# Kernel optimization log

Hardware: AMD Instinct MI355X
Metric: run time of the kernel (lower is better)

The kernel has to match this reference:

```python
import jax, jax.numpy as jnp
import numpy as np

B, S, D = 4, 2048, 256
H = 8
HD = D // H
FF = 1024
LEN_M1 = 513


def _layer_norm(x, gamma, beta, eps=1e-5):
    m = jnp.mean(x, axis=-1, keepdims=True)
    v = jnp.var(x, axis=-1, keepdims=True)
    return (x - m) * jax.lax.rsqrt(v + eps) * gamma + beta


def setup_inputs() -> dict:
    key = jax.random.key(0)
    ks = jax.random.split(key, 16)
    s = 0.02  # init scale for weights
    return {
        "src": jax.random.normal(ks[0], (B, S, D), dtype=jnp.float32),
        "Wq": jax.random.normal(ks[1], (D, D), dtype=jnp.float32) * s,
        "bq": jnp.zeros((D,), dtype=jnp.float32),
        "Wk": jax.random.normal(ks[2], (D, D), dtype=jnp.float32) * s,
        "bk": jnp.zeros((D,), dtype=jnp.float32),
        "Wv": jax.random.normal(ks[3], (D, D), dtype=jnp.float32) * s,
        "bv": jnp.zeros((D,), dtype=jnp.float32),
        "Wo": jax.random.normal(ks[4], (D, D), dtype=jnp.float32) * s,
        "bo": jnp.zeros((D,), dtype=jnp.float32),
        "W1": jax.random.normal(ks[5], (FF, D), dtype=jnp.float32) * s,
        "b1": jnp.zeros((FF,), dtype=jnp.float32),
        "W2": jax.random.normal(ks[6], (D, FF), dtype=jnp.float32) * s,
        "b2": jnp.zeros((D,), dtype=jnp.float32),
        "g1": jnp.ones((D,), dtype=jnp.float32),
        "be1": jnp.zeros((D,), dtype=jnp.float32),
        "g2": jnp.ones((D,), dtype=jnp.float32),
        "be2": jnp.zeros((D,), dtype=jnp.float32),
        "len_m1": LEN_M1,
    }


def reference(src, Wq, bq, Wk, bk, Wv, bv, Wo, bo, W1, b1, W2, b2, g1, be1, g2, be2, len_m1):
    Bb, Ss, Dd = src.shape
    hd = Dd // H
    # projections (torch Linear: x @ W.T + b), split heads -> [B,H,S,hd]
    q = (src @ Wq.T + bq).reshape(Bb, Ss, H, hd).transpose(0, 2, 1, 3)
    k = (src @ Wk.T + bk).reshape(Bb, Ss, H, hd).transpose(0, 2, 1, 3)
    v = (src @ Wv.T + bv).reshape(Bb, Ss, H, hd).transpose(0, 2, 1, 3)
    scores = jnp.einsum("bhqd,bhkd->bhqk", q, k) / np.sqrt(hd).astype(np.float32)
    # causal mask + global prefix block: masked where j > i OR (i < len_m1 and j >= len_m1)
    i = jnp.arange(Ss)[:, None]
    j = jnp.arange(Ss)[None, :]
    mask = (j > i) | ((i < len_m1) & (j >= len_m1))
    scores = jnp.where(mask, -jnp.inf, scores)
    attn = jax.nn.softmax(scores, axis=-1)
    ao = jnp.einsum("bhqk,bhkd->bhqd", attn, v).transpose(0, 2, 1, 3).reshape(Bb, Ss, Dd)
    src2 = _layer_norm(src + (ao @ Wo.T + bo), g1, be1)
    ff = jax.nn.gelu(src2 @ W1.T + b1, approximate=False) @ W2.T + b2
    return _layer_norm(src2 + ff, g2, be2)
```

## Files before the change

kernel.cpp:

```cpp
#include <hip/hip_runtime.h>
#include <math.h>

#define NB 4
#define NS 2048
#define ND 256
#define NH 8
#define NHD 32
#define NFF 1024
#define NM (NB*NS)
#define KPAD 40
#define VSP 72
#define VTP 72
#define AS 264
#define QSCALE 0.2550181657f

typedef __attribute__((ext_vector_type(4))) short short4v;
typedef __attribute__((ext_vector_type(8))) short short8v;
typedef __attribute__((ext_vector_type(4))) float f32x4;
typedef unsigned short us;

__device__ __forceinline__ us f2bf(float f){
  union { float f; unsigned u; } c; c.f = f;
  unsigned u = c.u + 0x7fffu + ((c.u >> 16) & 1u);
  return (us)(u >> 16);
}

__device__ __forceinline__ float wsum(float v){
  #pragma unroll
  for(int o=32;o>0;o>>=1) v += __shfl_xor(v,o);
  return v;
}

__global__ __launch_bounds__(256) void prep_kernel(
    const float* __restrict__ src,
    const float* __restrict__ Wq, const float* __restrict__ Wk, const float* __restrict__ Wv,
    const float* __restrict__ Wo, const float* __restrict__ W1, const float* __restrict__ W2,
    const float* __restrict__ bq,
    us* __restrict__ X, us* __restrict__ Wqkvb, us* __restrict__ Wob,
    us* __restrict__ W1b, us* __restrict__ W2b, float* __restrict__ bqs){
  unsigned bid = blockIdx.x;
  if (bid == 1408){ bqs[threadIdx.x] = bq[threadIdx.x]*QSCALE; return; }
  unsigned u = bid*256u + threadIdx.x;
  const float* sp; us* dp; float sc = 1.f;
  if (u < 262144u){ sp = src + (size_t)u*8; dp = X + (size_t)u*8; }
  else {
    unsigned v = u - 262144u;
    if      (v <  8192u){ sp = Wq + (size_t)v*8;            dp = Wqkvb + (size_t)v*8;            sc = QSCALE; }
    else if (v < 16384u){ sp = Wk + (size_t)(v- 8192u)*8;   dp = Wqkvb + 65536 + (size_t)(v- 8192u)*8; }
    else if (v < 24576u){ sp = Wv + (size_t)(v-16384u)*8;   dp = Wqkvb + 131072 + (size_t)(v-16384u)*8; }
    else if (v < 32768u){ sp = Wo + (size_t)(v-24576u)*8;   dp = Wob + (size_t)(v-24576u)*8; }
    else if (v < 65536u){ sp = W1 + (size_t)(v-32768u)*8;   dp = W1b + (size_t)(v-32768u)*8; }
    else               { sp = W2 + (size_t)(v-65536u)*8;    dp = W2b + (size_t)(v-65536u)*8; }
  }
  float4 a = *(const float4*)sp, b = *(const float4*)(sp+4);
  short8v o;
  o[0]=(short)f2bf(a.x*sc); o[1]=(short)f2bf(a.y*sc); o[2]=(short)f2bf(a.z*sc); o[3]=(short)f2bf(a.w*sc);
  o[4]=(short)f2bf(b.x*sc); o[5]=(short)f2bf(b.y*sc); o[6]=(short)f2bf(b.z*sc); o[7]=(short)f2bf(b.w*sc);
  *(short8v*)dp = o;
}

template<int KTOT, int EPI>
__global__ __launch_bounds__(256) void gemm_kernel(
    const us* __restrict__ A, const us* __restrict__ W,
    const float* __restrict__ bias0, const float* __restrict__ bias1, const float* __restrict__ bias2,
    const float* __restrict__ resid,
    us* __restrict__ outb, us* __restrict__ outv, float* __restrict__ outf){
  __shared__ us Asl[64*AS];
  const int t = threadIdx.x, l = t&63, wv = t>>6;
  const int lx = l&15, lw = l>>4;
  const int m0 = blockIdx.y*64;
  const int n0 = blockIdx.x*128 + wv*32;

  f32x4 acc[4][2];
  #pragma unroll
  for(int mb=0;mb<4;mb++)
    #pragma unroll
    for(int nb=0;nb<2;nb++) acc[mb][nb] = (f32x4){0.f,0.f,0.f,0.f};

  for (int kc = 0; kc < KTOT; kc += 256){
    __syncthreads();
    #pragma unroll
    for (int it=0; it<8; it++){
      int idx = it*256 + t;
      int r = idx>>5, c = idx&31;
      *(short8v*)&Asl[r*AS + c*8] = *(const short8v*)(A + (size_t)(m0+r)*KTOT + kc + c*8);
    }
    __syncthreads();
    short8v bf[2][8];
    #pragma unroll
    for (int nb=0; nb<2; nb++)
      #pragma unroll
      for (int ks=0; ks<8; ks++)
        bf[nb][ks] = *(const short8v*)(W + (size_t)(n0 + nb*16 + lx)*KTOT + kc + ks*32 + 8*lw);
    #pragma unroll
    for (int ks=0; ks<8; ks++){
      short8v af[4];
      #pragma unroll
      for (int mb=0; mb<4; mb++)
        af[mb] = *(const short8v*)&Asl[(mb*16+lx)*AS + ks*32 + 8*lw];
      #pragma unroll
      for (int mb=0; mb<4; mb++){
        acc[mb][0] = __builtin_amdgcn_mfma_f32_16x16x32_bf16(af[mb], bf[0][ks], acc[mb][0], 0,0,0);
        acc[mb][1] = __builtin_amdgcn_mfma_f32_16x16x32_bf16(af[mb], bf[1][ks], acc[mb][1], 0,0,0);
      }
    }
  }
  const int mr0 = m0 + 4*lw;
  #pragma unroll
  for (int nb=0; nb<2; nb++){
    int n = n0 + nb*16 + lx;
    if (EPI == 0){
      int seg = n >> 8, nn = n & 255;
      const float* bp = (seg==0) ? bias0 : (seg==1) ? bias1 : bias2;
      float bb = bp[nn];
      if (seg < 2){
        us* op = outb + (size_t)seg*((size_t)NM*ND) + nn;
        #pragma unroll
        for (int mb=0; mb<4; mb++)
          #pragma unroll
          for (int r=0; r<4; r++)
            op[(size_t)(mr0 + mb*16 + r)*ND] = f2bf(acc[mb][nb][r] + bb);
      } else {
        int hh = nn >> 5, dd = nn & 31;
        int bidx = mr0 >> 11;
        int s0 = mr0 & 2047;
        us* vp = outv + (((size_t)bidx*NH + hh)*NHD + dd)*NS;
        #pragma unroll
        for (int mb=0; mb<4; mb++){
          short4v v4;
          #pragma unroll
          for (int r=0; r<4; r++) v4[r] = (short)f2bf(acc[mb][nb][r] + bb);
          *(short4v*)(vp + s0 + mb*16) = v4;
        }
      }
    } else if (EPI == 1 || EPI == 3){
      float bb = bias0[n];
      #pragma unroll
      for (int mb=0; mb<4; mb++)
        #pragma unroll
        for (int r=0; r<4; r++){
          size_t off = (size_t)(mr0 + mb*16 + r)*ND + n;
          outf[off] = acc[mb][nb][r] + bb + resid[off];
        }
    } else {
      float bb = bias0[n];
      #pragma unroll
      for (int mb=0; mb<4; mb++)
        #pragma unroll
        for (int r=0; r<4; r++){
          float x = acc[mb][nb][r] + bb;
          float g = 0.5f*x*(1.f + erff(x*0.70710678118654752f));
          outb[(size_t)(mr0 + mb*16 + r)*NFF + n] = f2bf(g);
        }
    }
  }
}

__global__ __launch_bounds__(256) void ln_kernel(
    const float* __restrict__ Xin, const float* __restrict__ g, const float* __restrict__ be,
    us* __restrict__ outb, float* __restrict__ outf){
  const int t = threadIdx.x, lane = t&63, wv = t>>6;
  const int m0 = blockIdx.x*16;
  #pragma unroll
  for(int rr=0; rr<4; rr++){
    int r = m0 + wv*4 + rr;
    const float* xr = Xin + (size_t)r*ND;
    float x[4]; float s=0.f,q=0.f;
    #pragma unroll
    for(int k=0;k<4;k++){ x[k]=xr[lane+64*k]; s+=x[k]; q+=x[k]*x[k]; }
    s = wsum(s); q = wsum(q);
    float mean = s*(1.f/ND), var = q*(1.f/ND)-mean*mean;
    float rstd = rsqrtf(var+1e-5f);
    #pragma unroll
    for(int k=0;k<4;k++){
      int col = lane+64*k;
      float y = (x[k]-mean)*rstd*g[col] + be[col];
      if (outf) outf[(size_t)r*ND+col] = y;
      if (outb) outb[(size_t)r*ND+col] = f2bf(y);
    }
  }
}

template<bool MASK>
__device__ __forceinline__ void attn_tile(
    const us* __restrict__ Kl, const us* __restrict__ Vl, us* __restrict__ pw,
    const short8v qf, const int lx, const int lw, const int jt, const int qg,
    f32x4& acc0, f32x4& acc1, float& lsum){
  f32x4 s4[4];
  #pragma unroll
  for (int kb=0; kb<4; kb++){
    short8v kf = *(const short8v*)(Kl + (kb*16 + lx)*KPAD + 8*lw);
    f32x4 z = {0.f,0.f,0.f,0.f};
    s4[kb] = __builtin_amdgcn_mfma_f32_16x16x32_bf16(kf, qf, z, 0,0,0);
  }
  float p[16];
  #pragma unroll
  for (int kb=0; kb<4; kb++)
    #pragma unroll
    for (int r=0; r<4; r++){
      float x = exp2f(s4[kb][r]);
      if (MASK) x = ((jt + 16*kb + 4*lw + r) > qg) ? 0.f : x;
      p[kb*4+r] = x;
      lsum += x;
    }
  #pragma unroll
  for (int kb=0; kb<4; kb++){
    unsigned p0, p1;
    asm("v_cvt_pk_bf16_f32 %0, %1, %2" : "=v"(p0) : "v"(p[4*kb+0]), "v"(p[4*kb+1]));
    asm("v_cvt_pk_bf16_f32 %0, %1, %2" : "=v"(p1) : "v"(p[4*kb+2]), "v"(p[4*kb+3]));
    uint2 pk; pk.x = p0; pk.y = p1;
    *(uint2*)(pw + (size_t)lx*VTP + kb*16 + 4*lw) = pk;
  }
  #pragma unroll
  for (int c=0; c<2; c++){
    short8v pf  = *(const short8v*)(pw + (size_t)lx*VTP + 32*c + 8*lw);
    short8v vfL = *(const short8v*)(Vl + (size_t)( lx    )*VSP + 32*c + 8*lw);
    short8v vfH = *(const short8v*)(Vl + (size_t)(16+lx  )*VSP + 32*c + 8*lw);
    acc0 = __builtin_amdgcn_mfma_f32_16x16x32_bf16(vfL, pf, acc0, 0,0,0);
    acc1 = __builtin_amdgcn_mfma_f32_16x16x32_bf16(vfH, pf, acc1, 0,0,0);
  }
}

__global__ __launch_bounds__(256) void attn_kernel(
    const us* __restrict__ Q, const us* __restrict__ K,
    const us* __restrict__ Vt, us* __restrict__ AO){
  __shared__ us Klds[2][64*KPAD];
  __shared__ us Vs[2][32*VSP];
  __shared__ us Ex[4][16*VTP];

  const int t = threadIdx.x, l = t & 63, wv = t >> 6;
  const int lx = l & 15, lw = l >> 4;
  const int bid = blockIdx.x;
  const int qtile = 31 - (bid >> 5);
  const int bh = bid & 31;
  const int b = bh >> 3, h = bh & 7;
  const int qbase = qtile*64 + wv*16;
  const int qg = qbase + lx;

  const us* Qg = Q + ((size_t)b*NS)*ND + h*NHD;
  const us* Kg = K + ((size_t)b*NS)*ND + h*NHD;
  const us* Vg = Vt + (size_t)bh*NHD*NS;

  short8v qf = *(const short8v*)(Qg + (size_t)(qbase + lx)*ND + 8*lw);

  f32x4 acc0 = {0.f,0.f,0.f,0.f}, acc1 = {0.f,0.f,0.f,0.f};
  float lsum = 0.f;

  const int kr = t >> 2, kp = t & 3;
  const int vd = t >> 3, vp = t & 7;
  const int jmax = qtile*64;
  us* pw = &Ex[wv][0];

  {
    short8v k0 = *(const short8v*)(Kg + (size_t)kr*ND + kp*8);
    short8v v0 = *(const short8v*)(Vg + (size_t)vd*NS + vp*8);
    *(short8v*)&Klds[0][kr*KPAD + kp*8] = k0;
    *(short8v*)&Vs[0][vd*VSP + vp*8] = v0;
  }
  __syncthreads();

  int cur = 0;
  for (int jt = 0; jt < jmax; jt += 64){
    short8v kn = *(const short8v*)(Kg + (size_t)(jt + 64 + kr)*ND + kp*8);
    short8v vn = *(const short8v*)(Vg + (size_t)vd*NS + (jt + 64) + vp*8);
    attn_tile<false>(&Klds[cur][0], &Vs[cur][0], pw, qf, lx, lw, jt, qg, acc0, acc1, lsum);
    *(short8v*)&Klds[cur^1][kr*KPAD + kp*8] = kn;
    *(short8v*)&Vs[cur^1][vd*VSP + vp*8] = vn;
    __syncthreads();
    cur ^= 1;
  }
  attn_tile<true>(&Klds[cur][0], &Vs[cur][0], pw, qf, lx, lw, jmax, qg, acc0, acc1, lsum);

  float lt = lsum + __shfl_xor(lsum, 16);
  lt += __shfl_xor(lt, 32);
  float inv = 1.f / lt;
  float* ol = (float*)&Ex[wv][0];
  #pragma unroll
  for (int r=0;r<4;r++){
    ol[lx*36 +      4*lw + r] = acc0[r]*inv;
    ol[lx*36 + 16 + 4*lw + r] = acc1[r]*inv;
  }
  int rr = l >> 2, cc = l & 3;
  const float* op8 = &ol[rr*36 + cc*8];
  short8v o8;
  #pragma unroll
  for (int j=0;j<8;j++) o8[j] = (short)f2bf(op8[j]);
  *(short8v*)(AO + ((size_t)(b*NS + qbase + rr))*ND + h*NHD + cc*8) = o8;
}

extern "C" void kernel_launch(void* const* d_in, const int* in_sizes, int n_in,
                              void* d_out, int out_size, void* d_ws, size_t ws_size,
                              hipStream_t stream){
  const float* src = (const float*)d_in[0];
  const float* Wq  = (const float*)d_in[1];
  const float* bq  = (const float*)d_in[2];
  const float* Wk  = (const float*)d_in[3];
  const float* bk  = (const float*)d_in[4];
  const float* Wv  = (const float*)d_in[5];
  const float* bv  = (const float*)d_in[6];
  const float* Wo  = (const float*)d_in[7];
  const float* bo  = (const float*)d_in[8];
  const float* W1  = (const float*)d_in[9];
  const float* b1  = (const float*)d_in[10];
  const float* W2  = (const float*)d_in[11];
  const float* b2  = (const float*)d_in[12];
  const float* g1  = (const float*)d_in[13];
  const float* be1 = (const float*)d_in[14];
  const float* g2  = (const float*)d_in[15];
  const float* be2 = (const float*)d_in[16];

  const size_t MB = 1048576;
  unsigned char* w8 = (unsigned char*)d_ws;
  us* X     = (us*)(w8 + 0);
  us* Qb    = (us*)(w8 + 4*MB);
  us* Kb    = (us*)(w8 + 8*MB);
  us* Vtg   = (us*)(w8 + 12*MB);
  us* AO    = (us*)(w8 + 16*MB);
  us* S2b   = (us*)(w8 + 20*MB);
  us* FF    = (us*)(w8 + 24*MB);
  us* Wqkvb = (us*)(w8 + 40*MB);
  us* Wob   = (us*)(w8 + 40*MB + 384*1024);
  us* W1b   = (us*)(w8 + 40*MB + 512*1024);
  us* W2b   = (us*)(w8 + 40*MB + 1024*1024);
  float* bqs   = (float*)(w8 + 40*MB + 1536*1024);
  float* S2pre = (float*)(w8 + 42*MB);
  float* S2f   = (float*)(w8 + 50*MB);
  float* Ypre  = (float*)(w8 + 0);
  float* out = (float*)d_out;

  prep_kernel<<<1409, 256, 0, stream>>>(src, Wq,Wk,Wv,Wo,W1,W2, bq,
                                        X, Wqkvb, Wob, W1b, W2b, bqs);
  gemm_kernel<256,0><<<dim3(6,128), 256, 0, stream>>>(X, Wqkvb, bqs, bk, bv, nullptr, Qb, Vtg, nullptr);
  attn_kernel<<<1024, 256, 0, stream>>>(Qb, Kb, Vtg, AO);
  gemm_kernel<256,1><<<dim3(2,128), 256, 0, stream>>>(AO, Wob, bo, nullptr, nullptr, src, nullptr, nullptr, S2pre);
  ln_kernel<<<NM/16, 256, 0, stream>>>(S2pre, g1, be1, S2b, S2f);
  gemm_kernel<256,2><<<dim3(8,128), 256, 0, stream>>>(S2b, W1b, b1, nullptr, nullptr, nullptr, FF, nullptr, nullptr);
  gemm_kernel<1024,3><<<dim3(2,128), 256, 0, stream>>>(FF, W2b, b2, nullptr, nullptr, S2f, nullptr, nullptr, Ypre);
  ln_kernel<<<NM/16, 256, 0, stream>>>(Ypre, g2, be2, nullptr, out);
}
```

Baseline: 107.1 us.

## Feed softmax probabilities to PV MFMA from registers via permuted V layout

Removes the per-tile LDS round trip for the probability matrix: the P values stay in registers and are packed directly into the MFMA B operand. To make the register order match, V is written into LDS with a permuted key-column layout, split into two 4-element stores. The row-sum reduction is also rewritten as a pairwise tree. This removes LDS writes and reads plus their latency per tile, at the cost of more, smaller LDS stores for V.

```diff
diff --git a/kernel.cpp b/kernel.cpp
--- a/kernel.cpp
+++ b/kernel.cpp
@@ -183,7 +183,7 @@
 
 template<bool MASK>
 __device__ __forceinline__ void attn_tile(
-    const us* __restrict__ Kl, const us* __restrict__ Vl, us* __restrict__ pw,
+    const us* __restrict__ Kl, const us* __restrict__ Vl,
     const short8v qf, const int lx, const int lw, const int jt, const int qg,
     f32x4& acc0, f32x4& acc1, float& lsum){
   f32x4 s4[4];
@@ -201,23 +201,27 @@
       float x = exp2f(s4[kb][r]);
       if (MASK) x = ((jt + 16*kb + 4*lw + r) > qg) ? 0.f : x;
       p[kb*4+r] = x;
-      lsum += x;
-    }
-  #pragma unroll
-  for (int kb=0; kb<4; kb++){
-    unsigned p0, p1;
-    asm("v_cvt_pk_bf16_f32 %0, %1, %2" : "=v"(p0) : "v"(p[4*kb+0]), "v"(p[4*kb+1]));
-    asm("v_cvt_pk_bf16_f32 %0, %1, %2" : "=v"(p1) : "v"(p[4*kb+2]), "v"(p[4*kb+3]));
-    uint2 pk; pk.x = p0; pk.y = p1;
-    *(uint2*)(pw + (size_t)lx*VTP + kb*16 + 4*lw) = pk;
+    }
+  {
+    float a0=p[0]+p[1],   a1=p[2]+p[3],   a2=p[4]+p[5],   a3=p[6]+p[7];
+    float a4=p[8]+p[9],   a5=p[10]+p[11], a6=p[12]+p[13], a7=p[14]+p[15];
+    float b0=a0+a1, b1=a2+a3, b2=a4+a5, b3=a6+a7;
+    lsum += (b0+b1) + (b2+b3);
   }
   #pragma unroll
   for (int c=0; c<2; c++){
-    short8v pf  = *(const short8v*)(pw + (size_t)lx*VTP + 32*c + 8*lw);
-    short8v vfL = *(const short8v*)(Vl + (size_t)( lx    )*VSP + 32*c + 8*lw);
-    short8v vfH = *(const short8v*)(Vl + (size_t)(16+lx  )*VSP + 32*c + 8*lw);
-    acc0 = __builtin_amdgcn_mfma_f32_16x16x32_bf16(vfL, pf, acc0, 0,0,0);
-    acc1 = __builtin_amdgcn_mfma_f32_16x16x32_bf16(vfH, pf, acc1, 0,0,0);
+    unsigned w0,w1,w2,w3;
+    asm("v_cvt_pk_bf16_f32 %0, %1, %2" : "=v"(w0) : "v"(p[8*c+0]), "v"(p[8*c+1]));
+    asm("v_cvt_pk_bf16_f32 %0, %1, %2" : "=v"(w1) : "v"(p[8*c+2]), "v"(p[8*c+3]));
+    asm("v_cvt_pk_bf16_f32 %0, %1, %2" : "=v"(w2) : "v"(p[8*c+4]), "v"(p[8*c+5]));
+    asm("v_cvt_pk_bf16_f32 %0, %1, %2" : "=v"(w3) : "v"(p[8*c+6]), "v"(p[8*c+7]));
+    union { unsigned u[4]; short8v v; } pu;
+    pu.u[0]=w0; pu.u[1]=w1; pu.u[2]=w2; pu.u[3]=w3;
+    short8v pf = pu.v;
+    short8v aL = *(const short8v*)(Vl + (size_t)( lx    )*VSP + 32*c + 8*lw);
+    short8v aH = *(const short8v*)(Vl + (size_t)(16+lx  )*VSP + 32*c + 8*lw);
+    acc0 = __builtin_amdgcn_mfma_f32_16x16x32_bf16(aL, pf, acc0, 0,0,0);
+    acc1 = __builtin_amdgcn_mfma_f32_16x16x32_bf16(aH, pf, acc1, 0,0,0);
   }
 }
 
@@ -248,14 +252,16 @@
 
   const int kr = t >> 2, kp = t & 3;
   const int vd = t >> 3, vp = t & 7;
+  const int vS0 = 32*(vp>>2) + 16*(vp&1) + 4*((vp>>1)&1);
   const int jmax = qtile*64;
-  us* pw = &Ex[wv][0];
 
   {
     short8v k0 = *(const short8v*)(Kg + (size_t)kr*ND + kp*8);
     short8v v0 = *(const short8v*)(Vg + (size_t)vd*NS + vp*8);
     *(short8v*)&Klds[0][kr*KPAD + kp*8] = k0;
-    *(short8v*)&Vs[0][vd*VSP + vp*8] = v0;
+    short4v lo = {v0[0],v0[1],v0[2],v0[3]}, hi = {v0[4],v0[5],v0[6],v0[7]};
+    *(short4v*)&Vs[0][vd*VSP + vS0]     = lo;
+    *(short4v*)&Vs[0][vd*VSP + vS0 + 8] = hi;
   }
   __syncthreads();
 
@@ -263,13 +269,15 @@
   for (int jt = 0; jt < jmax; jt += 64){
     short8v kn = *(const short8v*)(Kg + (size_t)(jt + 64 + kr)*ND + kp*8);
     short8v vn = *(const short8v*)(Vg + (size_t)vd*NS + (jt + 64) + vp*8);
-    attn_tile<false>(&Klds[cur][0], &Vs[cur][0], pw, qf, lx, lw, jt, qg, acc0, acc1, lsum);
+    attn_tile<false>(&Klds[cur][0], &Vs[cur][0], qf, lx, lw, jt, qg, acc0, acc1, lsum);
     *(short8v*)&Klds[cur^1][kr*KPAD + kp*8] = kn;
-    *(short8v*)&Vs[cur^1][vd*VSP + vp*8] = vn;
+    short4v lo = {vn[0],vn[1],vn[2],vn[3]}, hi = {vn[4],vn[5],vn[6],vn[7]};
+    *(short4v*)&Vs[cur^1][vd*VSP + vS0]     = lo;
+    *(short4v*)&Vs[cur^1][vd*VSP + vS0 + 8] = hi;
     __syncthreads();
     cur ^= 1;
   }
-  attn_tile<true>(&Klds[cur][0], &Vs[cur][0], pw, qf, lx, lw, jmax, qg, acc0, acc1, lsum);
+  attn_tile<true>(&Klds[cur][0], &Vs[cur][0], qf, lx, lw, jmax, qg, acc0, acc1, lsum);
 
   float lt = lsum + __shfl_xor(lsum, 16);
   lt += __shfl_xor(lt, 32);
```

After: 106.5 us. Within noise of the previous version (-0.6%).
